# Performance work log

Measured on AMD Instinct MI355X. Metric: run time of the kernel, lower is better.

Reference implementation:

```python
import jax, jax.numpy as jnp
import numpy as np

B, T, C, H = 2, 2048, 1024, 16
D = C // H  # head dim = 64
EPS = 1e-5


def layernorm(x, g, b):
    mu = jnp.mean(x, axis=-1, keepdims=True)
    var = jnp.var(x, axis=-1, keepdims=True)
    return (x - mu) * jax.lax.rsqrt(var + EPS) * g + b


def setup_inputs() -> dict:
    key = jax.random.key(0)
    ks = jax.random.split(key, 8)
    init_scale = 0.25
    return {
        "x": jax.random.normal(ks[0], (B, T, C), dtype=jnp.float32),
        # weights stored [in, out] (transpose of torch Linear)
        "w_qkv": jax.random.normal(ks[1], (C, 3 * C), dtype=jnp.float32) * init_scale,
        "b_qkv": jnp.zeros((3 * C,), dtype=jnp.float32),
        "w_proj": jax.random.normal(ks[2], (C, C), dtype=jnp.float32) * init_scale,
        "b_proj": jnp.zeros((C,), dtype=jnp.float32),
        "ln1_g": jnp.ones((C,), dtype=jnp.float32),
        "ln1_b": jnp.zeros((C,), dtype=jnp.float32),
        "w_fc": jax.random.normal(ks[3], (C, 4 * C), dtype=jnp.float32) * init_scale,
        "b_fc": jnp.zeros((4 * C,), dtype=jnp.float32),
        "w_out": jax.random.normal(ks[4], (4 * C, C), dtype=jnp.float32) * init_scale,
        "b_out": jnp.zeros((C,), dtype=jnp.float32),
        "ln2_g": jnp.ones((C,), dtype=jnp.float32),
        "ln2_b": jnp.zeros((C,), dtype=jnp.float32),
    }


def reference(x, w_qkv, b_qkv, w_proj, b_proj, ln1_g, ln1_b,
              w_fc, b_fc, w_out, b_out, ln2_g, ln2_b):
    # ---- attention sub-block (pre-LN) ----
    h = layernorm(x, ln1_g, ln1_b)
    qkv = h @ w_qkv + b_qkv                      # [B,T,3C]
    q, k, v = jnp.split(qkv, 3, axis=-1)
    q = q.reshape(B, T, H, D)
    k = k.reshape(B, T, H, D)
    v = v.reshape(B, T, H, D)
    scores = jnp.einsum('bthd,bshd->bhts', q, k) * (1.0 / np.sqrt(D))
    attn = jax.nn.softmax(scores, axis=-1)       # full [B,H,T,T] as in source
    out = jnp.einsum('bhts,bshd->bthd', attn, v).reshape(B, T, C)
    x = x + out @ w_proj + b_proj
    # ---- MLP sub-block (pre-LN) ----
    h = layernorm(x, ln2_g, ln2_b)
    h = jax.nn.gelu(h @ w_fc + b_fc, approximate=False)  # torch nn.GELU default = exact
    x = x + h @ w_out + b_out
    return x
```

## Files before the change

kernel.cpp:

```cpp
#include <hip/hip_runtime.h>
#include <hip/hip_bf16.h>
#include <math.h>

#define DEVINL static __device__ __forceinline__

typedef _Float16 f16x8 __attribute__((ext_vector_type(8)));
typedef _Float16 f16x4 __attribute__((ext_vector_type(4)));
typedef float f32x4 __attribute__((ext_vector_type(4)));
typedef float f32x16 __attribute__((ext_vector_type(16)));

constexpr int TT = 2048, CC = 1024, HH = 16, DD = 64;
constexpr int HALF_Y = 2 * TT * CC;
constexpr int HALF_L = 2 * HH * TT;

DEVINL void gload_lds16(const void* g, void* s) {
  __builtin_amdgcn_global_load_lds(
      (const __attribute__((address_space(1))) void*)g,
      (__attribute__((address_space(3))) void*)s, 16, 0, 0);
}

DEVINL unsigned pkrtz(float a, float b) {
  typedef __fp16 hf2 __attribute__((ext_vector_type(2)));
  union { hf2 h; unsigned u; } c;
  c.h = __builtin_amdgcn_cvt_pkrtz(a, b);
  return c.u;
}

__global__ __launch_bounds__(256) void transpose_cast(
    const float* __restrict__ in, _Float16* __restrict__ out, int K, int N) {
  __shared__ float tile[32][33];
  int n0 = blockIdx.x * 32, k0 = blockIdx.y * 32;
  int tx = threadIdx.x & 31, ty = threadIdx.x >> 5;
  #pragma unroll
  for (int i = 0; i < 32; i += 8)
    tile[ty + i][tx] = in[(size_t)(k0 + ty + i) * N + n0 + tx];
  __syncthreads();
  #pragma unroll
  for (int i = 0; i < 32; i += 8)
    out[(size_t)(n0 + ty + i) * K + k0 + tx] = (_Float16)tile[tx][ty + i];
}

__global__ __launch_bounds__(256) void ln_cast(
    const float* __restrict__ x, const float* __restrict__ g,
    const float* __restrict__ bta, _Float16* __restrict__ out) {
  int row = blockIdx.x, t = threadIdx.x;
  float4 v = ((const float4*)(x + (size_t)row * CC))[t];
  float s = v.x + v.y + v.z + v.w;
  float s2 = v.x * v.x + v.y * v.y + v.z * v.z + v.w * v.w;
  #pragma unroll
  for (int o = 32; o >= 1; o >>= 1) { s += __shfl_xor(s, o); s2 += __shfl_xor(s2, o); }
  __shared__ float ss[4], ssq[4];
  int w = t >> 6;
  if ((t & 63) == 0) { ss[w] = s; ssq[w] = s2; }
  __syncthreads();
  s = ss[0] + ss[1] + ss[2] + ss[3];
  s2 = ssq[0] + ssq[1] + ssq[2] + ssq[3];
  float mu = s * (1.0f / CC);
  float rs = rsqrtf(s2 * (1.0f / CC) - mu * mu + 1e-5f);
  float4 gv = ((const float4*)g)[t];
  float4 bv = ((const float4*)bta)[t];
  f16x4 o4;
  o4[0] = (_Float16)((v.x - mu) * rs * gv.x + bv.x);
  o4[1] = (_Float16)((v.y - mu) * rs * gv.y + bv.y);
  o4[2] = (_Float16)((v.z - mu) * rs * gv.z + bv.z);
  o4[3] = (_Float16)((v.w - mu) * rs * gv.w + bv.w);
  ((f16x4*)(out + (size_t)row * CC))[t] = o4;
}

template <int EPI, int N, int K, int BN>
__global__ __launch_bounds__(256) void gemm_bt(
    const _Float16* __restrict__ A, const _Float16* __restrict__ Bt,
    const float* __restrict__ bias, const float* __restrict__ res,
    void* __restrict__ outp) {
  constexpr int NWN = BN / 64;
  constexpr int MI = 2 * NWN;
  __shared__ __align__(16) _Float16 As[128 * 64];
  __shared__ __align__(16) _Float16 Bs[BN * 64];
  const int bm0 = blockIdx.y * 128, bn0 = blockIdx.x * BN;
  const int t = threadIdx.x, w = t >> 6, l = t & 63, lg = l >> 4, lr = l & 15;
  const int wr = w / NWN, wc = w % NWN;
  const int srow = t >> 3, sc = t & 7;
  f32x4 acc[MI][4] = {};
  for (int k0 = 0; k0 < K; k0 += 64) {
    #pragma unroll
    for (int q = 0; q < 4; ++q) {
      int row = q * 32 + srow;
      int gc = sc ^ (row & 7);
      gload_lds16(A + (size_t)(bm0 + row) * K + k0 + gc * 8, As + row * 64 + sc * 8);
    }
    #pragma unroll
    for (int q = 0; q < BN / 32; ++q) {
      int row = q * 32 + srow;
      int gc = sc ^ (row & 7);
      gload_lds16(Bt + (size_t)(bn0 + row) * K + k0 + gc * 8, Bs + row * 64 + sc * 8);
    }
    __syncthreads();
    #pragma unroll
    for (int ks = 0; ks < 2; ++ks) {
      f16x8 af[MI], bfr[4];
      #pragma unroll
      for (int mi = 0; mi < MI; ++mi) {
        int row = wr * (16 * MI) + mi * 16 + lr;
        af[mi] = *(const f16x8*)(As + row * 64 + (((ks * 4 + lg) ^ (row & 7)) << 3));
      }
      #pragma unroll
      for (int ni = 0; ni < 4; ++ni) {
        int row = wc * 64 + ni * 16 + lr;
        bfr[ni] = *(const f16x8*)(Bs + row * 64 + (((ks * 4 + lg) ^ (row & 7)) << 3));
      }
      #pragma unroll
      for (int mi = 0; mi < MI; ++mi)
        #pragma unroll
        for (int ni = 0; ni < 4; ++ni)
          acc[mi][ni] = __builtin_amdgcn_mfma_f32_16x16x32_f16(af[mi], bfr[ni], acc[mi][ni], 0, 0, 0);
    }
    __syncthreads();
  }
  #pragma unroll
  for (int mi = 0; mi < MI; ++mi) {
    #pragma unroll
    for (int ni = 0; ni < 4; ++ni) {
      int gc = bn0 + wc * 64 + ni * 16 + lr;
      float bv = bias[gc];
      #pragma unroll
      for (int r = 0; r < 4; ++r) {
        int gr = bm0 + wr * (16 * MI) + mi * 16 + lg * 4 + r;
        float v = acc[mi][ni][r] + bv;
        if constexpr (EPI == 1) {
          float gl = 0.5f * v * (1.0f + erff(v * 0.70710678118654752f));
          ((_Float16*)outp)[(size_t)gr * N + gc] = (_Float16)gl;
        } else {
          ((float*)outp)[(size_t)gr * N + gc] = res[(size_t)gr * N + gc] + v;
        }
      }
    }
  }
}

__global__ __launch_bounds__(256) void gemm_qkv(
    const _Float16* __restrict__ A, const _Float16* __restrict__ Bt,
    const float* __restrict__ bias,
    _Float16* __restrict__ qo, _Float16* __restrict__ ko,
    _Float16* __restrict__ vt) {
  __shared__ __align__(16) _Float16 As[128 * 64];
  __shared__ __align__(16) _Float16 Bs[128 * 64];
  const int bm0 = blockIdx.y * 128, bn0 = blockIdx.x * 128;
  const int t = threadIdx.x, w = t >> 6, l = t & 63, lg = l >> 4, lr = l & 15;
  const int wr = w >> 1, wc = w & 1;
  const int srow = t >> 3, sc = t & 7;
  f32x4 acc[4][4] = {};
  for (int k0 = 0; k0 < 1024; k0 += 64) {
    #pragma unroll
    for (int q = 0; q < 4; ++q) {
      int row = q * 32 + srow;
      int gc = sc ^ (row & 7);
      gload_lds16(A + (size_t)(bm0 + row) * 1024 + k0 + gc * 8, As + row * 64 + sc * 8);
      gload_lds16(Bt + (size_t)(bn0 + row) * 1024 + k0 + gc * 8, Bs + row * 64 + sc * 8);
    }
    __syncthreads();
    #pragma unroll
    for (int ks = 0; ks < 2; ++ks) {
      f16x8 af[4], bfr[4];
      #pragma unroll
      for (int mi = 0; mi < 4; ++mi) {
        int row = wr * 64 + mi * 16 + lr;
        af[mi] = *(const f16x8*)(As + row * 64 + (((ks * 4 + lg) ^ (row & 7)) << 3));
      }
      #pragma unroll
      for (int ni = 0; ni < 4; ++ni) {
        int row = wc * 64 + ni * 16 + lr;
        bfr[ni] = *(const f16x8*)(Bs + row * 64 + (((ks * 4 + lg) ^ (row & 7)) << 3));
      }
      #pragma unroll
      for (int mi = 0; mi < 4; ++mi)
        #pragma unroll
        for (int ni = 0; ni < 4; ++ni)
          acc[mi][ni] = __builtin_amdgcn_mfma_f32_16x16x32_f16(af[mi], bfr[ni], acc[mi][ni], 0, 0, 0);
    }
    __syncthreads();
  }
  const float QSCL = 0.125f * 1.44269504f;
  #pragma unroll
  for (int mi = 0; mi < 4; ++mi) {
    #pragma unroll
    for (int ni = 0; ni < 4; ++ni) {
      int gc = bn0 + wc * 64 + ni * 16 + lr;
      float bv = bias[gc];
      int sec = gc >> 10, cc = gc & 1023;
      #pragma unroll
      for (int r = 0; r < 4; ++r) {
        int gr = bm0 + wr * 64 + mi * 16 + lg * 4 + r;
        float v = acc[mi][ni][r] + bv;
        if (sec == 0) {
          qo[(size_t)gr * 1024 + cc] = (_Float16)(v * QSCL);
        } else if (sec == 1) {
          ko[(size_t)gr * 1024 + cc] = (_Float16)v;
        } else {
          int hh = cc >> 6, dd = cc & 63;
          int bb = gr >> 11, tk = gr & (TT - 1);
          vt[(((size_t)bb * HH + hh) * DD + dd) * TT + tk] = (_Float16)v;
        }
      }
    }
  }
}

__global__ __launch_bounds__(256, 4) void flash_attn(
    const _Float16* __restrict__ qg, const _Float16* __restrict__ kg,
    const _Float16* __restrict__ vt, _Float16* __restrict__ yp,
    float* __restrict__ Lp) {
  const int qt0 = blockIdx.x * 128, h = blockIdx.y;
  const int b = blockIdx.z & 1, half = blockIdx.z >> 1;
  const int kvbeg = half * (TT / 2), kvend = kvbeg + TT / 2;
  const int t = threadIdx.x, w = t >> 6, l = t & 63;
  const int l31 = l & 31, hi = l >> 5;
  __shared__ __align__(16) _Float16 Ks[2][64 * 64];
  __shared__ __align__(16) _Float16 VTs[2][64 * 64];
  const int srow = t >> 3, sc = t & 7;
  const int gc0 = sc ^ (srow & 7) ^ ((srow >> 3) & 7);
  const int gc1 = sc ^ (srow & 7) ^ (((srow >> 3) + 4) & 7);
  const _Float16* kg_r = kg + ((size_t)b * TT + srow) * CC + h * DD;
  const _Float16* vt_r = vt + (((size_t)b * HH + h) * DD + srow) * TT;
  const int dst0 = srow * 64 + sc * 8;

  f16x8 qf[4];
  {
    const _Float16* qp = qg + ((size_t)(b * TT + qt0 + w * 32 + l31)) * CC + h * DD + hi * 8;
    #pragma unroll
    for (int ks = 0; ks < 4; ++ks) qf[ks] = *(const f16x8*)(qp + ks * 16);
  }
  const int rx = l31 & 7, ry = (l31 >> 3) & 7;
  int swk[2], swv[2];
  #pragma unroll
  for (int sub = 0; sub < 2; ++sub) swk[sub] = rx ^ ((sub * 4 + ry) & 7);
  swv[0] = rx ^ ry;
  swv[1] = rx ^ ((4 + ry) & 7);

  f32x16 o0 = {}, o1 = {};
  float osum = 0.0f, mrow = -3.0e38f;

  auto STAGE = [&](int bufi, int kv0) {
    gload_lds16(kg_r + (size_t)kv0 * CC + gc0 * 8, Ks[bufi] + dst0);
    gload_lds16(kg_r + (size_t)(kv0 + 32) * CC + gc1 * 8, Ks[bufi] + 2048 + dst0);
    gload_lds16(vt_r + kv0 + gc0 * 8, VTs[bufi] + dst0);
    gload_lds16(vt_r + 32 * TT + kv0 + gc1 * 8, VTs[bufi] + 2048 + dst0);
  };
  STAGE(0, kvbeg);
  __syncthreads();
  int cur = 0;
  for (int kv0 = kvbeg; kv0 < kvend; kv0 += 64) {
    if (kv0 + 64 < kvend) STAGE(cur ^ 1, kv0 + 64);
    const _Float16* Kc = Ks[cur];
    const _Float16* Vc = VTs[cur];
    #pragma unroll
    for (int sub = 0; sub < 2; ++sub) {
      f32x16 s = {};
      const int krow = (sub * 32 + l31) * 64;
      __builtin_amdgcn_s_setprio(1);
      #pragma unroll
      for (int ks = 0; ks < 4; ++ks) {
        f16x8 kf = *(const f16x8*)(Kc + krow + (((ks * 2 + hi) ^ swk[sub]) << 3));
        s = __builtin_amdgcn_mfma_f32_32x32x16_f16(kf, qf[ks], s, 0, 0, 0);
      }
      __builtin_amdgcn_s_setprio(0);
      float m01 = fmaxf(fmaxf(s[0], s[1]), fmaxf(s[2], s[3]));
      float m23 = fmaxf(fmaxf(s[4], s[5]), fmaxf(s[6], s[7]));
      float m45 = fmaxf(fmaxf(s[8], s[9]), fmaxf(s[10], s[11]));
      float m67 = fmaxf(fmaxf(s[12], s[13]), fmaxf(s[14], s[15]));
      float m16v = fmaxf(fmaxf(m01, m23), fmaxf(m45, m67));
      int ok = (m16v <= mrow + 8.0f) ? 1 : 0;
      if (!__all(ok)) {
        float mo = fmaxf(m16v, __shfl_xor(m16v, 32));
        float mn = fmaxf(mrow, mo);
        float corr = exp2f(mrow - mn);
        mrow = mn;
        #pragma unroll
        for (int r = 0; r < 16; ++r) { o0[r] *= corr; o1[r] *= corr; }
        osum *= corr;
      }
      float p[16];
      float psum = 0.0f;
      #pragma unroll
      for (int r = 0; r < 16; ++r) { p[r] = exp2f(s[r] - mrow); psum += p[r]; }
      osum += psum;
      unsigned W[8], X[8];
      #pragma unroll
      for (int i = 0; i < 8; ++i) {
        W[i] = pkrtz(p[2 * i], p[2 * i + 1]);
        X[i] = __shfl_xor(W[i], 32);
      }
      union { unsigned u[4]; f16x8 v; } bp[2];
      #pragma unroll
      for (int s2 = 0; s2 < 2; ++s2) {
        bp[s2].u[0] = hi ? X[4 * s2 + 2] : W[4 * s2 + 0];
        bp[s2].u[1] = hi ? X[4 * s2 + 3] : W[4 * s2 + 1];
        bp[s2].u[2] = hi ? W[4 * s2 + 2] : X[4 * s2 + 0];
        bp[s2].u[3] = hi ? W[4 * s2 + 3] : X[4 * s2 + 1];
      }
      __builtin_amdgcn_s_setprio(1);
      #pragma unroll
      for (int s2 = 0; s2 < 2; ++s2) {
        int c = sub * 4 + s2 * 2 + hi;
        {
          f16x8 vf = *(const f16x8*)(Vc + l31 * 64 + ((c ^ swv[0]) << 3));
          o0 = __builtin_amdgcn_mfma_f32_32x32x16_f16(vf, bp[s2].v, o0, 0, 0, 0);
        }
        {
          f16x8 vf = *(const f16x8*)(Vc + (32 + l31) * 64 + ((c ^ swv[1]) << 3));
          o1 = __builtin_amdgcn_mfma_f32_32x32x16_f16(vf, bp[s2].v, o1, 0, 0, 0);
        }
      }
      __builtin_amdgcn_s_setprio(0);
    }
    __syncthreads();
    cur ^= 1;
  }
  osum += __shfl_xor(osum, 32);
  float rinv = 1.0f / osum;
  const int qrow = qt0 + w * 32 + l31;
  _Float16* ob = yp + (size_t)half * HALF_Y + ((size_t)(b * TT + qrow)) * CC + h * DD;
  #pragma unroll
  for (int i = 0; i < 4; ++i) {
    int col0 = 8 * i + 4 * hi;
    uint2 v0, v1;
    v0.x = pkrtz(o0[4 * i + 0] * rinv, o0[4 * i + 1] * rinv);
    v0.y = pkrtz(o0[4 * i + 2] * rinv, o0[4 * i + 3] * rinv);
    v1.x = pkrtz(o1[4 * i + 0] * rinv, o1[4 * i + 1] * rinv);
    v1.y = pkrtz(o1[4 * i + 2] * rinv, o1[4 * i + 3] * rinv);
    *(uint2*)(ob + col0) = v0;
    *(uint2*)(ob + 32 + col0) = v1;
  }
  if (hi == 0)
    Lp[(size_t)half * HALF_L + ((size_t)b * HH + h) * TT + qrow] =
        mrow + log2f(osum);
}

__global__ __launch_bounds__(256) void attn_combine(
    const _Float16* __restrict__ yp, const float* __restrict__ Lp,
    _Float16* __restrict__ att) {
  int bt = blockIdx.x;
  int b = bt >> 11, tt = bt & (TT - 1);
  int tid = threadIdx.x;
  int h = tid >> 4;
  size_t li = ((size_t)b * HH + h) * TT + tt;
  float L0 = Lp[li], L1 = Lp[HALF_L + li];
  float m = fmaxf(L0, L1);
  float w0 = exp2f(L0 - m), w1 = exp2f(L1 - m);
  float rs = 1.0f / (w0 + w1);
  w0 *= rs; w1 *= rs;
  f16x4 a = ((const f16x4*)(yp + (size_t)bt * CC))[tid];
  f16x4 c = ((const f16x4*)(yp + HALF_Y + (size_t)bt * CC))[tid];
  f16x4 o;
  #pragma unroll
  for (int i = 0; i < 4; ++i)
    o[i] = (_Float16)(w0 * (float)a[i] + w1 * (float)c[i]);
  ((f16x4*)(att + (size_t)bt * CC))[tid] = o;
}

extern "C" void kernel_launch(void* const* d_in, const int* in_sizes, int n_in,
                              void* d_out, int out_size, void* d_ws, size_t ws_size,
                              hipStream_t stream) {
  const float* x      = (const float*)d_in[0];
  const float* w_qkv  = (const float*)d_in[1];
  const float* b_qkv  = (const float*)d_in[2];
  const float* w_proj = (const float*)d_in[3];
  const float* b_proj = (const float*)d_in[4];
  const float* ln1_g  = (const float*)d_in[5];
  const float* ln1_b  = (const float*)d_in[6];
  const float* w_fc   = (const float*)d_in[7];
  const float* b_fc   = (const float*)d_in[8];
  const float* w_out  = (const float*)d_in[9];
  const float* b_out  = (const float*)d_in[10];
  const float* ln2_g  = (const float*)d_in[11];
  const float* ln2_b  = (const float*)d_in[12];

  char* ws = (char*)d_ws;
  _Float16* wqkv_t = (_Float16*)(ws);
  _Float16* wproj_t= (_Float16*)(ws + 6291456);
  _Float16* wfc_t  = (_Float16*)(ws + 8388608);
  _Float16* wout_t = (_Float16*)(ws + 16777216);
  _Float16* hslot  = (_Float16*)(ws + 25165824);
  _Float16* qbuf   = (_Float16*)(ws + 33554432);
  _Float16* kbuf   = (_Float16*)(ws + 41943040);
  _Float16* vtbuf  = (_Float16*)(ws + 50331648);
  _Float16* tbuf   = (_Float16*)(ws + 33554432);
  float*    x1     = (float*)(ws + 67108864);
  _Float16* ypart  = (_Float16*)(ws + 83886080);
  float*    Lpart  = (float*)(ws + 100663296);

  transpose_cast<<<dim3(96, 32), 256, 0, stream>>>(w_qkv, wqkv_t, 1024, 3072);
  transpose_cast<<<dim3(32, 32), 256, 0, stream>>>(w_proj, wproj_t, 1024, 1024);
  transpose_cast<<<dim3(128, 32), 256, 0, stream>>>(w_fc, wfc_t, 1024, 4096);
  transpose_cast<<<dim3(32, 128), 256, 0, stream>>>(w_out, wout_t, 4096, 1024);

  ln_cast<<<4096, 256, 0, stream>>>(x, ln1_g, ln1_b, hslot);
  gemm_qkv<<<dim3(24, 32), 256, 0, stream>>>(hslot, wqkv_t, b_qkv, qbuf, kbuf, vtbuf);
  flash_attn<<<dim3(16, 16, 4), 256, 0, stream>>>(qbuf, kbuf, vtbuf, ypart, Lpart);
  attn_combine<<<4096, 256, 0, stream>>>(ypart, Lpart, hslot);
  gemm_bt<2, 1024, 1024, 64><<<dim3(16, 32), 256, 0, stream>>>(hslot, wproj_t, b_proj, x, x1);
  ln_cast<<<4096, 256, 0, stream>>>(x1, ln2_g, ln2_b, hslot);
  gemm_bt<1, 4096, 1024, 128><<<dim3(32, 32), 256, 0, stream>>>(hslot, wfc_t, b_fc, nullptr, tbuf);
  gemm_bt<2, 1024, 4096, 64><<<dim3(16, 32), 256, 0, stream>>>(tbuf, wout_t, b_out, x1, (float*)d_out);
}
```

Measured before the change: 300.3 us.

## Double-buffer LDS in proj/out GEMMs and use fast sigmoid GELU approximation

Adds an optional double-buffered LDS pipeline to gemm_bt. It prefetches the next K tile with global_load_lds while the MFMAs run on the current one, using a vmcnt wait and raw barriers, and enables it for the proj and MLP-out GEMMs. It also replaces the exact erf GELU in the FC epilogue with a sigmoid-based approximation using exp2 and rcp. The approximation trades exactness for fewer ALU ops and may exceed the tolerance of the exact GELU reference. Double buffering doubles LDS use for those kernels, which may reduce occupancy.

After: 286.0 us. 1.05x faster.

```diff
diff --git a/kernel.cpp b/kernel.cpp
--- a/kernel.cpp
+++ b/kernel.cpp
@@ -24,6 +24,11 @@
   union { hf2 h; unsigned u; } c;
   c.h = __builtin_amdgcn_cvt_pkrtz(a, b);
   return c.u;
+}
+
+DEVINL float fast_gelu(float v) {
+  float z = v * (2.302208214f + 0.102945116f * v * v);
+  return v * __builtin_amdgcn_rcpf(1.0f + exp2f(-z));
 }
 
 __global__ __launch_bounds__(256) void transpose_cast(
@@ -67,46 +72,50 @@
   ((f16x4*)(out + (size_t)row * CC))[t] = o4;
 }
 
-template <int EPI, int N, int K, int BN>
+template <int EPI, int N, int K, int BN, int DBUF>
 __global__ __launch_bounds__(256) void gemm_bt(
     const _Float16* __restrict__ A, const _Float16* __restrict__ Bt,
     const float* __restrict__ bias, const float* __restrict__ res,
     void* __restrict__ outp) {
   constexpr int NWN = BN / 64;
   constexpr int MI = 2 * NWN;
-  __shared__ __align__(16) _Float16 As[128 * 64];
-  __shared__ __align__(16) _Float16 Bs[BN * 64];
+  constexpr int NB = DBUF ? 2 : 1;
+  constexpr int NLOADS = 4 + BN / 32;
+  __shared__ __align__(16) _Float16 As[NB][128 * 64];
+  __shared__ __align__(16) _Float16 Bs[NB][BN * 64];
   const int bm0 = blockIdx.y * 128, bn0 = blockIdx.x * BN;
   const int t = threadIdx.x, w = t >> 6, l = t & 63, lg = l >> 4, lr = l & 15;
   const int wr = w / NWN, wc = w % NWN;
   const int srow = t >> 3, sc = t & 7;
   f32x4 acc[MI][4] = {};
-  for (int k0 = 0; k0 < K; k0 += 64) {
+
+  auto STAGE = [&](int bi, int k0) {
     #pragma unroll
     for (int q = 0; q < 4; ++q) {
       int row = q * 32 + srow;
       int gc = sc ^ (row & 7);
-      gload_lds16(A + (size_t)(bm0 + row) * K + k0 + gc * 8, As + row * 64 + sc * 8);
+      gload_lds16(A + (size_t)(bm0 + row) * K + k0 + gc * 8, As[bi] + row * 64 + sc * 8);
     }
     #pragma unroll
     for (int q = 0; q < BN / 32; ++q) {
       int row = q * 32 + srow;
       int gc = sc ^ (row & 7);
-      gload_lds16(Bt + (size_t)(bn0 + row) * K + k0 + gc * 8, Bs + row * 64 + sc * 8);
-    }
-    __syncthreads();
+      gload_lds16(Bt + (size_t)(bn0 + row) * K + k0 + gc * 8, Bs[bi] + row * 64 + sc * 8);
+    }
+  };
+  auto COMPUTE = [&](const _Float16* Ac, const _Float16* Bc) {
     #pragma unroll
     for (int ks = 0; ks < 2; ++ks) {
       f16x8 af[MI], bfr[4];
       #pragma unroll
       for (int mi = 0; mi < MI; ++mi) {
         int row = wr * (16 * MI) + mi * 16 + lr;
-        af[mi] = *(const f16x8*)(As + row * 64 + (((ks * 4 + lg) ^ (row & 7)) << 3));
+        af[mi] = *(const f16x8*)(Ac + row * 64 + (((ks * 4 + lg) ^ (row & 7)) << 3));
       }
       #pragma unroll
       for (int ni = 0; ni < 4; ++ni) {
         int row = wc * 64 + ni * 16 + lr;
-        bfr[ni] = *(const f16x8*)(Bs + row * 64 + (((ks * 4 + lg) ^ (row & 7)) << 3));
+        bfr[ni] = *(const f16x8*)(Bc + row * 64 + (((ks * 4 + lg) ^ (row & 7)) << 3));
       }
       #pragma unroll
       for (int mi = 0; mi < MI; ++mi)
@@ -114,8 +123,32 @@
         for (int ni = 0; ni < 4; ++ni)
           acc[mi][ni] = __builtin_amdgcn_mfma_f32_16x16x32_f16(af[mi], bfr[ni], acc[mi][ni], 0, 0, 0);
     }
-    __syncthreads();
-  }
+  };
+
+  if constexpr (DBUF) {
+    STAGE(0, 0);
+    int cur = 0;
+    for (int k0 = 0; k0 < K; k0 += 64) {
+      if (k0 + 64 < K) {
+        STAGE(cur ^ 1, k0 + 64);
+        asm volatile("s_waitcnt vmcnt(%0)" :: "i"(NLOADS) : "memory");
+      } else {
+        asm volatile("s_waitcnt vmcnt(0)" ::: "memory");
+      }
+      __builtin_amdgcn_s_barrier();
+      COMPUTE(As[cur], Bs[cur]);
+      __builtin_amdgcn_s_barrier();
+      cur ^= 1;
+    }
+  } else {
+    for (int k0 = 0; k0 < K; k0 += 64) {
+      STAGE(0, k0);
+      __syncthreads();
+      COMPUTE(As[0], Bs[0]);
+      __syncthreads();
+    }
+  }
+
   #pragma unroll
   for (int mi = 0; mi < MI; ++mi) {
     #pragma unroll
@@ -127,8 +160,7 @@
         int gr = bm0 + wr * (16 * MI) + mi * 16 + lg * 4 + r;
         float v = acc[mi][ni][r] + bv;
         if constexpr (EPI == 1) {
-          float gl = 0.5f * v * (1.0f + erff(v * 0.70710678118654752f));
-          ((_Float16*)outp)[(size_t)gr * N + gc] = (_Float16)gl;
+          ((_Float16*)outp)[(size_t)gr * N + gc] = (_Float16)fast_gelu(v);
         } else {
           ((float*)outp)[(size_t)gr * N + gc] = res[(size_t)gr * N + gc] + v;
         }
@@ -397,8 +429,8 @@
   gemm_qkv<<<dim3(24, 32), 256, 0, stream>>>(hslot, wqkv_t, b_qkv, qbuf, kbuf, vtbuf);
   flash_attn<<<dim3(16, 16, 4), 256, 0, stream>>>(qbuf, kbuf, vtbuf, ypart, Lpart);
   attn_combine<<<4096, 256, 0, stream>>>(ypart, Lpart, hslot);
-  gemm_bt<2, 1024, 1024, 64><<<dim3(16, 32), 256, 0, stream>>>(hslot, wproj_t, b_proj, x, x1);
+  gemm_bt<2, 1024, 1024, 64, 1><<<dim3(16, 32), 256, 0, stream>>>(hslot, wproj_t, b_proj, x, x1);
   ln_cast<<<4096, 256, 0, stream>>>(x1, ln2_g, ln2_b, hslot);
-  gemm_bt<1, 4096, 1024, 128><<<dim3(32, 32), 256, 0, stream>>>(hslot, wfc_t, b_fc, nullptr, tbuf);
-  gemm_bt<2, 1024, 4096, 64><<<dim3(16, 32), 256, 0, stream>>>(tbuf, wout_t, b_out, x1, (float*)d_out);
-}
+  gemm_bt<1, 4096, 1024, 128, 0><<<dim3(32, 32), 256, 0, stream>>>(hslot, wfc_t, b_fc, nullptr, tbuf);
+  gemm_bt<2, 1024, 4096, 64, 1><<<dim3(16, 32), 256, 0, stream>>>(tbuf, wout_t, b_out, x1, (float*)d_out);
+}
```
